# Optimization experiments

Hardware: AMD Instinct MI355X
Metric: run time of the kernel (lower is better)

The kernel has to match this reference:

```python
import jax, jax.numpy as jnp
import numpy as np

NUM_HEADS = 16

def setup_inputs() -> dict:
    key = jax.random.key(0)
    ks = jax.random.split(key, 6)
    b, t, d = 2, 2048, 1024
    s = 0.02
    return {
        "x": jax.random.normal(ks[0], (b, t, d), jnp.float32),
        "Wq": jax.random.normal(ks[1], (d, d), jnp.float32) * s,
        "Wk": jax.random.normal(ks[2], (d, d), jnp.float32) * s,
        "Wv": jax.random.normal(ks[3], (d, d), jnp.float32) * s,
        "Wo": jax.random.normal(ks[4], (d, d), jnp.float32) * s,
        "bo": jnp.zeros((d,), jnp.float32),
    }

def reference(x, Wq, Wk, Wv, Wo, bo):
    b, t, d = x.shape
    h = NUM_HEADS
    hd = d // h  # head_dim = d_out / num_heads
    # torch nn.Linear: y = x @ W.T (qkv_bias=False)
    def split_heads(y):
        return y.reshape(b, t, h, hd).transpose(0, 2, 1, 3)  # [b,h,t,hd]
    q = split_heads(x @ Wq.T)
    k = split_heads(x @ Wk.T)
    v = split_heads(x @ Wv.T)
    scale = 1.0 / jnp.sqrt(jnp.asarray(hd, x.dtype))
    # NOTE: original forward computes but never applies the causal mask or dropout
    scores = jnp.einsum('bhqd,bhkd->bhqk', q, k) * scale
    attn = jax.nn.softmax(scores, axis=-1)
    ctx = jnp.einsum('bhqk,bhkd->bhqd', attn, v)
    ctx = ctx.transpose(0, 2, 1, 3).reshape(b, t, d)
    return ctx @ Wo.T + bo
```

## Files before the change

kernel.cpp:

```cpp
#include <hip/hip_runtime.h>
#include <hip/hip_bf16.h>
#include <math.h>
#include <stdint.h>
#include <string.h>

#define TSEQ 2048
#define DMODEL 1024
#define NH 16
#define HD 64
#define BROWS 4096
#define BH 32

typedef __attribute__((ext_vector_type(8))) short short8;
typedef __attribute__((ext_vector_type(4))) float floatx4;

#define MFMA16 __builtin_amdgcn_mfma_f32_16x16x32_bf16
#define SWZ8(r, q) ((((q) ^ ((r) & 7)) * 8))

#define QSCALE 0.18033688011112042f

__device__ __forceinline__ unsigned short bf16_rne(float f) {
    uint32_t u = __float_as_uint(f);
    u += 0x7FFFu + ((u >> 16) & 1u);
    return (unsigned short)(u >> 16);
}

__device__ __forceinline__ uint32_t pack_bf16x2(float a, float b) {
    __hip_bfloat162 h = __float22bfloat162_rn(float2{a, b});
    uint32_t r;
    memcpy(&r, &h, 4);
    return r;
}

__device__ __forceinline__ void split_bf16(float f, short& hi, short& lo) {
    uint32_t u = __float_as_uint(f);
    hi = (short)(u >> 16);
    float hif = __uint_as_float(u & 0xFFFF0000u);
    lo = (short)bf16_rne(f - hif);
}

__device__ __forceinline__ void async16(const void* g, void* l) {
    __builtin_amdgcn_global_load_lds(
        (__attribute__((address_space(1))) const uint32_t*)g,
        (__attribute__((address_space(3))) uint32_t*)l, 16, 0, 0);
}

struct PackArgs {
    const float4* x;
    ushort4* xb;
    const float4* w[3];
    ushort4* wb[3];
    const float4* wo;
    ushort4* woh;
    ushort4* wol;
};
__global__ __launch_bounds__(256) void pack_all(PackArgs a) {
    const int y = blockIdx.y;
    const int base = blockIdx.x * 256 + threadIdx.x;
    if (y == 0) {
#pragma unroll
        for (int it = 0; it < 4; ++it) {
            int i = base + it * 262144;
            float4 f = a.x[i];
            a.xb[i] = make_ushort4(bf16_rne(f.x), bf16_rne(f.y),
                                   bf16_rne(f.z), bf16_rne(f.w));
        }
    } else if (y <= 3) {
        int w = y - 1;
        float4 f = a.w[w][base];
        a.wb[w][base] = make_ushort4(bf16_rne(f.x), bf16_rne(f.y),
                                     bf16_rne(f.z), bf16_rne(f.w));
    } else {
        float4 f = a.wo[base];
        short h0, l0, h1, l1, h2, l2, h3, l3;
        split_bf16(f.x, h0, l0); split_bf16(f.y, h1, l1);
        split_bf16(f.z, h2, l2); split_bf16(f.w, h3, l3);
        a.woh[base] = make_ushort4(h0, h1, h2, h3);
        a.wol[base] = make_ushort4(l0, l1, l2, l3);
    }
}

#define QSTAGE(DB, K0)                                                          \
    {                                                                           \
        _Pragma("unroll")                                                       \
        for (int j = 0; j < 8; ++j) {                                           \
            int idx = wave * 8 + j;                                             \
            int sub = idx & 15;                                                 \
            const short* s = (idx < 16) ? Asrc : Bsrc;                          \
            short* d = (idx < 16) ? sA[DB] : sB[DB];                            \
            async16(s + (size_t)(sub * 8 + srow) * K + (K0) + soff, d + sub * 512); \
        }                                                                       \
    }

__global__ __launch_bounds__(256) void gemm_qkv(
    const short* __restrict__ Xb,
    const short* __restrict__ Bq, const short* __restrict__ Bk,
    const short* __restrict__ Bv,
    short* __restrict__ Qo, short* __restrict__ Ko, short* __restrict__ Vo) {
    __shared__ short sA[2][128 * 64];
    __shared__ short sB[2][128 * 64];
    const int K = DMODEL;

    const int tid = threadIdx.x;
    const int lane = tid & 63, wave = tid >> 6;
    const int quad = lane >> 4, col = lane & 15;

    const int lin = blockIdx.y * 24 + blockIdx.x;
    const int xcd = lin & 7, j8 = lin >> 3;
    const int bxp = 3 * xcd + (j8 % 3);
    const int byp = j8 / 3;
    const int m0 = byp * 128, n0 = bxp * 128;
    const int which = n0 >> 10;
    const int nn0 = n0 & 1023;
    const int wm = wave >> 1, wn = wave & 1;

    const short* B = (which == 0) ? Bq : (which == 1) ? Bk : Bv;
    const short* Asrc = Xb + (size_t)m0 * K;
    const short* Bsrc = B + (size_t)nn0 * K;

    const int srow = lane >> 3;
    const int soff = (((lane & 7) ^ srow) * 8);

    floatx4 acc[4][4] = {};

    QSTAGE(0, 0);
    for (int t = 0; t < 16; ++t) {
        const int db = t & 1;
        if (t < 15) {
            QSTAGE(db ^ 1, (t + 1) * 64);
            asm volatile("s_waitcnt vmcnt(8)" ::: "memory");
        } else {
            asm volatile("s_waitcnt vmcnt(0)" ::: "memory");
        }
        __builtin_amdgcn_s_barrier();

#pragma unroll
        for (int s2 = 0; s2 < 2; ++s2) {
            short8 a_b[4], b_b[4];
#pragma unroll
            for (int mi = 0; mi < 4; ++mi) {
                int r = wm * 64 + mi * 16 + col;
                a_b[mi] = *(const short8*)&sA[db][r * 64 + SWZ8(r, s2 * 4 + quad)];
            }
#pragma unroll
            for (int ni = 0; ni < 4; ++ni) {
                int r = wn * 64 + ni * 16 + col;
                b_b[ni] = *(const short8*)&sB[db][r * 64 + SWZ8(r, s2 * 4 + quad)];
            }
            __builtin_amdgcn_s_setprio(1);
            if (which == 2) {
#pragma unroll
                for (int mi = 0; mi < 4; ++mi)
#pragma unroll
                    for (int ni = 0; ni < 4; ++ni)
                        acc[mi][ni] = MFMA16(a_b[mi], b_b[ni], acc[mi][ni], 0, 0, 0);
            } else {
#pragma unroll
                for (int mi = 0; mi < 4; ++mi)
#pragma unroll
                    for (int ni = 0; ni < 4; ++ni)
                        acc[mi][ni] = MFMA16(b_b[ni], a_b[mi], acc[mi][ni], 0, 0, 0);
            }
            __builtin_amdgcn_s_setprio(0);
        }
        __builtin_amdgcn_s_barrier();
    }

    const int mb = m0 + wm * 64;
    const int nlb = nn0 + wn * 64;
    if (which == 2) {
#pragma unroll
        for (int ni = 0; ni < 4; ++ni) {
            int n = nlb + ni * 16 + col;
            int h = n >> 6, hd = n & 63;
#pragma unroll
            for (int mi = 0; mi < 4; ++mi) {
                int m4 = mb + mi * 16 + quad * 4;
                int b = m4 >> 11, t0 = m4 & 2047;
                int sw = (t0 & 32) | ((t0 & 12) << 1) | ((t0 & 16) >> 2);
                int tsw = (t0 & ~63) | ((((sw >> 3) ^ (hd & 7)) << 3) | (sw & 7));
                size_t row = ((size_t)(b * NH + h) * HD + hd) * TSEQ;
                *(ushort4*)&Vo[row + tsw] =
                    make_ushort4(bf16_rne(acc[mi][ni][0]), bf16_rne(acc[mi][ni][1]),
                                 bf16_rne(acc[mi][ni][2]), bf16_rne(acc[mi][ni][3]));
            }
        }
    } else {
        short* O = (which == 0) ? Qo : Ko;
        const float sc = (which == 0) ? QSCALE : 1.0f;
#pragma unroll
        for (int mi = 0; mi < 4; ++mi) {
            int m = mb + mi * 16 + col;
            int b = m >> 11, t = m & 2047;
#pragma unroll
            for (int ni = 0; ni < 4; ++ni) {
                int n = nlb + ni * 16 + quad * 4;
                int h = n >> 6, hd = n & 63;
                int hds = (which == 1) ? ((((hd >> 3) ^ (t & 7)) << 3) | (hd & 7)) : hd;
                size_t idx = ((size_t)(b * NH + h) * TSEQ + t) * HD + hds;
                *(ushort4*)&O[idx] =
                    make_ushort4(bf16_rne(acc[mi][ni][0] * sc), bf16_rne(acc[mi][ni][1] * sc),
                                 bf16_rne(acc[mi][ni][2] * sc), bf16_rne(acc[mi][ni][3] * sc));
            }
        }
    }
}

#define QK_U(DB, U, S)                                                          \
    {                                                                           \
        __builtin_amdgcn_s_setprio(1);                                          \
        _Pragma("unroll")                                                       \
        for (int k4 = 0; k4 < 4; ++k4) {                                        \
            short8 kf0 = *(const short8*)(kb0 + (DB) * 8192 + (U) * 4096 + k4 * 1024); \
            short8 kf1 = *(const short8*)(kb1 + (DB) * 8192 + (U) * 4096 + k4 * 1024); \
            S[k4] = MFMA16(kf0, qf[0], S[k4], 0, 0, 0);                         \
            S[k4] = MFMA16(kf1, qf[1], S[k4], 0, 0, 0);                         \
        }                                                                       \
        __builtin_amdgcn_s_setprio(0);                                          \
    }

#define EXPPACK_C(S, C, PFW)                                                    \
    {                                                                           \
        float p0 = __builtin_amdgcn_exp2f(S[2 * (C)][0]);                       \
        float p1 = __builtin_amdgcn_exp2f(S[2 * (C)][1]);                       \
        float p2 = __builtin_amdgcn_exp2f(S[2 * (C)][2]);                       \
        float p3 = __builtin_amdgcn_exp2f(S[2 * (C)][3]);                       \
        float p4 = __builtin_amdgcn_exp2f(S[2 * (C) + 1][0]);                   \
        float p5 = __builtin_amdgcn_exp2f(S[2 * (C) + 1][1]);                   \
        float p6 = __builtin_amdgcn_exp2f(S[2 * (C) + 1][2]);                   \
        float p7 = __builtin_amdgcn_exp2f(S[2 * (C) + 1][3]);                   \
        PFW.w[0] = pack_bf16x2(p0, p1);                                         \
        PFW.w[1] = pack_bf16x2(p2, p3);                                         \
        PFW.w[2] = pack_bf16x2(p4, p5);                                         \
        PFW.w[3] = pack_bf16x2(p6, p7);                                         \
    }

#define PV_C(DB, U, C, PFW)                                                     \
    {                                                                           \
        const short* vbc = (C) ? vb1 : vb0;                                     \
        __builtin_amdgcn_s_setprio(1);                                          \
        lacc = MFMA16(ones.v, PFW.v, lacc, 0, 0, 0);                            \
        _Pragma("unroll")                                                       \
        for (int ni = 0; ni < 4; ++ni) {                                        \
            short8 vf = *(const short8*)(vbc + (DB) * 8192 + (U) * 4096 + ni * 1024); \
            O[ni] = MFMA16(vf, PFW.v, O[ni], 0, 0, 0);                          \
        }                                                                       \
        __builtin_amdgcn_s_setprio(0);                                          \
    }

typedef union { short8 v; uint32_t w[4]; } pfu;

#define ATTN_COMPUTE(DB)                                                        \
    {                                                                           \
        floatx4 sa[4] = {};                                                     \
        QK_U(DB, 0, sa);                                                        \
        pfu pfA0, pfA1;                                                         \
        EXPPACK_C(sa, 0, pfA0);                                                 \
        EXPPACK_C(sa, 1, pfA1);                                                 \
        floatx4 sb[4] = {};                                                     \
        QK_U(DB, 1, sb);                                                        \
              \
        pfu pfB0, pfB1;                                                         \
        PV_C(DB, 0, 0, pfA0);                                                   \
        EXPPACK_C(sb, 0, pfB0);                                                 \
        PV_C(DB, 0, 1, pfA1);                                                   \
        EXPPACK_C(sb, 1, pfB1);                                                 \
        PV_C(DB, 1, 0, pfB0);                                                   \
        PV_C(DB, 1, 1, pfB1);                                                   \
    }

#define ASTAGE(LB)                                                              \
    {                                                                           \
        async16(g0, (LB) + 0 * 512);                                            \
        async16(g1, (LB) + 1 * 512);                                            \
        async16(g2, (LB) + 2 * 512);                                            \
        async16(g3, (LB) + 3 * 512);                                            \
        g0 += ktstep; g1 += ktstep; g2 += ktstep; g3 += ktstep;                 \
    }

__global__ __launch_bounds__(512, 4) void attn_bf16(
    const short* __restrict__ Qb, const short* __restrict__ Kb,
    const short* __restrict__ Vb, short* __restrict__ Cb) {
    __shared__ short sK[2][2][64 * 64];
    __shared__ short sV[2][2][64 * 64];

    const int tid = threadIdx.x;
    const int lane = tid & 63, wave = tid >> 6;
    const int quad = lane >> 4, col = lane & 15;
    const int qt = blockIdx.x, bh = blockIdx.y;
    const size_t bhoff = (size_t)bh * TSEQ * HD;

    const size_t qrow = (size_t)(qt * 128 + wave * 16 + col) * HD;
    short8 qf[2];
#pragma unroll
    for (int c = 0; c < 2; ++c)
        qf[c] = *(const short8*)&Qb[bhoff + qrow + c * 32 + quad * 8];

    const int srow = lane >> 3;
    const int schunk = (lane & 7) * 8;

    const int isV = wave >> 2;
    const int tl = (wave >> 1) & 1;
    const int sb = (wave & 1) * 4;

    const short *g0, *g1, *g2, *g3;
    size_t ktstep;
    if (!isV) {
        g0 = Kb + bhoff + (size_t)(tl * 64 + (sb + 0) * 8 + srow) * HD + schunk;
        g1 = Kb + bhoff + (size_t)(tl * 64 + (sb + 1) * 8 + srow) * HD + schunk;
        g2 = Kb + bhoff + (size_t)(tl * 64 + (sb + 2) * 8 + srow) * HD + schunk;
        g3 = Kb + bhoff + (size_t)(tl * 64 + (sb + 3) * 8 + srow) * HD + schunk;
        ktstep = (size_t)128 * HD;
    } else {
        g0 = Vb + bhoff + (size_t)((sb + 0) * 8 + srow) * TSEQ + tl * 64 + schunk;
        g1 = Vb + bhoff + (size_t)((sb + 1) * 8 + srow) * TSEQ + tl * 64 + schunk;
        g2 = Vb + bhoff + (size_t)((sb + 2) * 8 + srow) * TSEQ + tl * 64 + schunk;
        g3 = Vb + bhoff + (size_t)((sb + 3) * 8 + srow) * TSEQ + tl * 64 + schunk;
        ktstep = 128;
    }
    short* lb0_ = isV ? &sV[0][tl][sb * 512] : &sK[0][tl][sb * 512];
    short* lb1_ = isV ? &sV[1][tl][sb * 512] : &sK[1][tl][sb * 512];

    const int ch0 = ((quad ^ (col & 7)) << 3);
    const int ch1 = (((4 + quad) ^ (col & 7)) << 3);
    const short* kb0 = &sK[0][0][col * 64 + ch0];
    const short* kb1 = &sK[0][0][col * 64 + ch1];
    const short* vb0 = &sV[0][0][col * 64 + ch0];
    const short* vb1 = &sV[0][0][col * 64 + ch1];

    union { short8 v; short s[8]; } ones;
#pragma unroll
    for (int j = 0; j < 8; ++j) ones.s[j] = (short)0x3F80;

    floatx4 lacc = {};
    floatx4 O[4] = {};

    ASTAGE(lb0_);

    for (int kt2 = 0; kt2 < 8; ++kt2) {
        ASTAGE(lb1_);
        asm volatile("s_waitcnt vmcnt(4)" ::: "memory");
        __builtin_amdgcn_s_barrier();
        ATTN_COMPUTE(0);
        __builtin_amdgcn_s_barrier();

        if (kt2 < 7) {
            ASTAGE(lb0_);
            asm volatile("s_waitcnt vmcnt(4)" ::: "memory");
        } else {
            asm volatile("s_waitcnt vmcnt(0)" ::: "memory");
        }
        __builtin_amdgcn_s_barrier();
        ATTN_COMPUTE(1);
        __builtin_amdgcn_s_barrier();
    }

    const float inv = 1.0f / lacc[0];

    const int b = bh >> 4, h = bh & 15;
    const int trow = qt * 128 + wave * 16 + col;
    const size_t obase = (size_t)(b * TSEQ + trow) * DMODEL + h * 64;
#pragma unroll
    for (int ni = 0; ni < 4; ++ni) {
        uint2 pk;
        pk.x = pack_bf16x2(O[ni][0] * inv, O[ni][1] * inv);
        pk.y = pack_bf16x2(O[ni][2] * inv, O[ni][3] * inv);
        *(uint2*)&Cb[obase + ni * 16 + quad * 4] = pk;
    }
}

#define OSTAGE(DB, K0)                                                          \
    {                                                                           \
        _Pragma("unroll")                                                       \
        for (int j = 0; j < 8; ++j) {                                           \
            int idx = wave * 8 + j;                                             \
            int buf = (idx < 16) ? 0 : (idx < 24) ? 1 : 2;                      \
            int sub = (buf == 0) ? idx : (buf == 1) ? idx - 16 : idx - 24;      \
            const short* s = (buf == 0) ? Asrc : (buf == 1) ? Bhsrc : Blsrc;    \
            short* d = (buf == 0) ? sA[DB] : (buf == 1) ? sBh[DB] : sBl[DB];    \
            async16(s + (size_t)(sub * 8 + srow) * K + (K0) + soff, d + sub * 512); \
        }                                                                       \
    }

__global__ __launch_bounds__(256) void gemm_out(
    const short* __restrict__ Ab,
    const short* __restrict__ Bh, const short* __restrict__ Bl,
    const float* __restrict__ bias, float* __restrict__ Of) {
    __shared__ short sA[2][128 * 64];
    __shared__ short sBh[2][64 * 64];
    __shared__ short sBl[2][64 * 64];
    const int K = DMODEL, N = DMODEL;

    const int tid = threadIdx.x;
    const int lane = tid & 63, wave = tid >> 6;
    const int quad = lane >> 4, col = lane & 15;

    const int lin = blockIdx.y * 16 + blockIdx.x;
    const int xcd = lin & 7, j8 = lin >> 3;
    const int bxp = 2 * xcd + (j8 & 1);
    const int byp = j8 >> 1;
    const int m0 = byp * 128, n0 = bxp * 64;
    const int wm = wave >> 1, wn = wave & 1;

    const short* Asrc = Ab + (size_t)m0 * K;
    const short* Bhsrc = Bh + (size_t)n0 * K;
    const short* Blsrc = Bl + (size_t)n0 * K;
    const int srow = lane >> 3;
    const int soff = (((lane & 7) ^ srow) * 8);

    floatx4 acc[4][2] = {};

    OSTAGE(0, 0);
    for (int t = 0; t < 16; ++t) {
        const int db = t & 1;
        if (t < 15) {
            OSTAGE(db ^ 1, (t + 1) * 64);
            asm volatile("s_waitcnt vmcnt(8)" ::: "memory");
        } else {
            asm volatile("s_waitcnt vmcnt(0)" ::: "memory");
        }
        __builtin_amdgcn_s_barrier();

#pragma unroll
        for (int s2 = 0; s2 < 2; ++s2) {
            short8 a_b[4], b_h[2], b_l[2];
#pragma unroll
            for (int mi = 0; mi < 4; ++mi) {
                int r = wm * 64 + mi * 16 + col;
                a_b[mi] = *(const short8*)&sA[db][r * 64 + SWZ8(r, s2 * 4 + quad)];
            }
#pragma unroll
            for (int ni = 0; ni < 2; ++ni) {
                int r = wn * 32 + ni * 16 + col;
                b_h[ni] = *(const short8*)&sBh[db][r * 64 + SWZ8(r, s2 * 4 + quad)];
                b_l[ni] = *(const short8*)&sBl[db][r * 64 + SWZ8(r, s2 * 4 + quad)];
            }
            __builtin_amdgcn_s_setprio(1);
#pragma unroll
            for (int mi = 0; mi < 4; ++mi)
#pragma unroll
                for (int ni = 0; ni < 2; ++ni) {
                    acc[mi][ni] = MFMA16(b_h[ni], a_b[mi], acc[mi][ni], 0, 0, 0);
                    acc[mi][ni] = MFMA16(b_l[ni], a_b[mi], acc[mi][ni], 0, 0, 0);
                }
            __builtin_amdgcn_s_setprio(0);
        }
        __builtin_amdgcn_s_barrier();
    }

    const int mb = m0 + wm * 64, nb = n0 + wn * 32;
#pragma unroll
    for (int mi = 0; mi < 4; ++mi) {
        int m = mb + mi * 16 + col;
#pragma unroll
        for (int ni = 0; ni < 2; ++ni) {
            int n = nb + ni * 16 + quad * 4;
            float4 bv = *(const float4*)&bias[n];
            float4 o = make_float4(acc[mi][ni][0] + bv.x, acc[mi][ni][1] + bv.y,
                                   acc[mi][ni][2] + bv.z, acc[mi][ni][3] + bv.w);
            *(float4*)&Of[(size_t)m * N + n] = o;
        }
    }
}

extern "C" void kernel_launch(void* const* d_in, const int* in_sizes, int n_in,
                              void* d_out, int out_size, void* d_ws, size_t ws_size,
                              hipStream_t stream) {
    const float* x  = (const float*)d_in[0];
    const float* Wq = (const float*)d_in[1];
    const float* Wk = (const float*)d_in[2];
    const float* Wv = (const float*)d_in[3];
    const float* Wo = (const float*)d_in[4];
    const float* bo = (const float*)d_in[5];
    float* out = (float*)d_out;

    const size_t NX = (size_t)BROWS * DMODEL;
    const size_t NW = (size_t)DMODEL * DMODEL;
    short* p = (short*)d_ws;
    short *xb = p;
    short *wqb = xb + NX;
    short *wkb = wqb + NW;
    short *wvb = wkb + NW;
    short *woh = wvb + NW; short *wol = woh + NW;
    short *qb = wol + NW;
    short *kb = qb + NX;
    short *vb = kb + NX;
    short *cb = vb + NX;

    PackArgs pa;
    pa.x = (const float4*)x; pa.xb = (ushort4*)xb;
    pa.w[0] = (const float4*)Wq; pa.wb[0] = (ushort4*)wqb;
    pa.w[1] = (const float4*)Wk; pa.wb[1] = (ushort4*)wkb;
    pa.w[2] = (const float4*)Wv; pa.wb[2] = (ushort4*)wvb;
    pa.wo = (const float4*)Wo; pa.woh = (ushort4*)woh; pa.wol = (ushort4*)wol;
    pack_all<<<dim3(1024, 5), dim3(256), 0, stream>>>(pa);

    gemm_qkv<<<dim3(3 * DMODEL / 128, BROWS / 128), dim3(256), 0, stream>>>(
        xb, wqb, wkb, wvb, qb, kb, vb);

    attn_bf16<<<dim3(TSEQ / 128, BH), dim3(512), 0, stream>>>(qb, kb, vb, cb);

    gemm_out<<<dim3(DMODEL / 64, BROWS / 128), dim3(256), 0, stream>>>(cb, woh, wol, bo, out);
}
```

Before: 186.7 us.

## Load K fragments directly from global memory and stage only V in LDS

The attention kernel stops staging K tiles in shared memory. Each wave now reads its K MFMA fragments straight from global memory into registers, while V keeps its LDS double buffer, now loaded by all eight waves at two chunks each. Block indices are also remapped so that blocks sharing a batch-head land on the same XCD, which should improve L2 reuse of K and V. This cuts LDS traffic and halves LDS use, at the cost of redundant global/L2 K reads across waves, exposed global load latency inside the compute loop, and stricter vmcnt(0) waits that reduce overlap of prefetch with compute.

```diff
diff --git a/kernel.cpp b/kernel.cpp
--- a/kernel.cpp
+++ b/kernel.cpp
@@ -206,18 +206,7 @@
     }
 }
 
-#define QK_U(DB, U, S)                                                          \
-    {                                                                           \
-        __builtin_amdgcn_s_setprio(1);                                          \
-        _Pragma("unroll")                                                       \
-        for (int k4 = 0; k4 < 4; ++k4) {                                        \
-            short8 kf0 = *(const short8*)(kb0 + (DB) * 8192 + (U) * 4096 + k4 * 1024); \
-            short8 kf1 = *(const short8*)(kb1 + (DB) * 8192 + (U) * 4096 + k4 * 1024); \
-            S[k4] = MFMA16(kf0, qf[0], S[k4], 0, 0, 0);                         \
-            S[k4] = MFMA16(kf1, qf[1], S[k4], 0, 0, 0);                         \
-        }                                                                       \
-        __builtin_amdgcn_s_setprio(0);                                          \
-    }
+typedef union { short8 v; uint32_t w[4]; } pfu;
 
 #define EXPPACK_C(S, C, PFW)                                                    \
     {                                                                           \
@@ -248,18 +237,39 @@
         __builtin_amdgcn_s_setprio(0);                                          \
     }
 
-typedef union { short8 v; uint32_t w[4]; } pfu;
-
-#define ATTN_COMPUTE(DB)                                                        \
-    {                                                                           \
+#define KLOAD_U(U, KF)                                                          \
+    {                                                                           \
+        _Pragma("unroll")                                                       \
+        for (int k4 = 0; k4 < 4; ++k4) {                                        \
+            KF[2 * k4]     = *(const short8*)(gk0 + (U) * 4096 + k4 * 1024);    \
+            KF[2 * k4 + 1] = *(const short8*)(gk1 + (U) * 4096 + k4 * 1024);    \
+        }                                                                       \
+    }
+
+#define QK_FROM(KF, S)                                                          \
+    {                                                                           \
+        __builtin_amdgcn_s_setprio(1);                                          \
+        _Pragma("unroll")                                                       \
+        for (int k4 = 0; k4 < 4; ++k4) {                                        \
+            S[k4] = MFMA16(KF[2 * k4], qf[0], S[k4], 0, 0, 0);                  \
+            S[k4] = MFMA16(KF[2 * k4 + 1], qf[1], S[k4], 0, 0, 0);              \
+        }                                                                       \
+        __builtin_amdgcn_s_setprio(0);                                          \
+    }
+
+#define ATTN_COMPUTE_G(DB)                                                      \
+    {                                                                           \
+        short8 ka[8];                                                           \
+        KLOAD_U(0, ka);                                                         \
         floatx4 sa[4] = {};                                                     \
-        QK_U(DB, 0, sa);                                                        \
+        QK_FROM(ka, sa);                                                        \
+        short8 kb_[8];                                                          \
+        KLOAD_U(1, kb_);                 \
         pfu pfA0, pfA1;                                                         \
         EXPPACK_C(sa, 0, pfA0);                                                 \
         EXPPACK_C(sa, 1, pfA1);                                                 \
         floatx4 sb[4] = {};                                                     \
-        QK_U(DB, 1, sb);                                                        \
-              \
+        QK_FROM(kb_, sb);                                                       \
         pfu pfB0, pfB1;                                                         \
         PV_C(DB, 0, 0, pfA0);                                                   \
         EXPPACK_C(sb, 0, pfB0);                                                 \
@@ -269,25 +279,26 @@
         PV_C(DB, 1, 1, pfB1);                                                   \
     }
 
-#define ASTAGE(LB)                                                              \
-    {                                                                           \
-        async16(g0, (LB) + 0 * 512);                                            \
-        async16(g1, (LB) + 1 * 512);                                            \
-        async16(g2, (LB) + 2 * 512);                                            \
-        async16(g3, (LB) + 3 * 512);                                            \
-        g0 += ktstep; g1 += ktstep; g2 += ktstep; g3 += ktstep;                 \
+#define VSTAGE(D0, D1)                                                          \
+    {                                                                           \
+        async16(gv0, D0);                                                       \
+        async16(gv1, D1);                                                       \
+        gv0 += 128; gv1 += 128;                                                 \
     }
 
 __global__ __launch_bounds__(512, 4) void attn_bf16(
     const short* __restrict__ Qb, const short* __restrict__ Kb,
     const short* __restrict__ Vb, short* __restrict__ Cb) {
-    __shared__ short sK[2][2][64 * 64];
-    __shared__ short sV[2][2][64 * 64];
+    __shared__ short sV[2][2][4096];
 
     const int tid = threadIdx.x;
     const int lane = tid & 63, wave = tid >> 6;
     const int quad = lane >> 4, col = lane & 15;
-    const int qt = blockIdx.x, bh = blockIdx.y;
+
+    const int lin = blockIdx.y * 16 + blockIdx.x;
+    const int xcd = lin & 7, j8 = lin >> 3;
+    const int qt = j8 & 15;
+    const int bh = 4 * xcd + (j8 >> 4);
     const size_t bhoff = (size_t)bh * TSEQ * HD;
 
     const size_t qrow = (size_t)(qt * 128 + wave * 16 + col) * HD;
@@ -299,32 +310,21 @@
     const int srow = lane >> 3;
     const int schunk = (lane & 7) * 8;
 
-    const int isV = wave >> 2;
-    const int tl = (wave >> 1) & 1;
-    const int sb = (wave & 1) * 4;
-
-    const short *g0, *g1, *g2, *g3;
-    size_t ktstep;
-    if (!isV) {
-        g0 = Kb + bhoff + (size_t)(tl * 64 + (sb + 0) * 8 + srow) * HD + schunk;
-        g1 = Kb + bhoff + (size_t)(tl * 64 + (sb + 1) * 8 + srow) * HD + schunk;
-        g2 = Kb + bhoff + (size_t)(tl * 64 + (sb + 2) * 8 + srow) * HD + schunk;
-        g3 = Kb + bhoff + (size_t)(tl * 64 + (sb + 3) * 8 + srow) * HD + schunk;
-        ktstep = (size_t)128 * HD;
-    } else {
-        g0 = Vb + bhoff + (size_t)((sb + 0) * 8 + srow) * TSEQ + tl * 64 + schunk;
-        g1 = Vb + bhoff + (size_t)((sb + 1) * 8 + srow) * TSEQ + tl * 64 + schunk;
-        g2 = Vb + bhoff + (size_t)((sb + 2) * 8 + srow) * TSEQ + tl * 64 + schunk;
-        g3 = Vb + bhoff + (size_t)((sb + 3) * 8 + srow) * TSEQ + tl * 64 + schunk;
-        ktstep = 128;
-    }
-    short* lb0_ = isV ? &sV[0][tl][sb * 512] : &sK[0][tl][sb * 512];
-    short* lb1_ = isV ? &sV[1][tl][sb * 512] : &sK[1][tl][sb * 512];
+    const int n0_ = wave * 2, n1_ = n0_ + 1;
+    const int tl0 = n0_ >> 3, sb0 = n0_ & 7;
+    const int tl1 = n1_ >> 3, sb1 = n1_ & 7;
+    const short* gv0 = Vb + bhoff + (size_t)(sb0 * 8 + srow) * TSEQ + tl0 * 64 + schunk;
+    const short* gv1 = Vb + bhoff + (size_t)(sb1 * 8 + srow) * TSEQ + tl1 * 64 + schunk;
+    short* vd0_0 = &sV[0][tl0][sb0 * 512];
+    short* vd0_1 = &sV[0][tl1][sb1 * 512];
+    short* vd1_0 = &sV[1][tl0][sb0 * 512];
+    short* vd1_1 = &sV[1][tl1][sb1 * 512];
 
     const int ch0 = ((quad ^ (col & 7)) << 3);
     const int ch1 = (((4 + quad) ^ (col & 7)) << 3);
-    const short* kb0 = &sK[0][0][col * 64 + ch0];
-    const short* kb1 = &sK[0][0][col * 64 + ch1];
+    const short* gk0 = Kb + bhoff + col * HD + ch0;
+    const short* gk1 = Kb + bhoff + col * HD + ch1;
+
     const short* vb0 = &sV[0][0][col * 64 + ch0];
     const short* vb1 = &sV[0][0][col * 64 + ch1];
 
@@ -335,23 +335,23 @@
     floatx4 lacc = {};
     floatx4 O[4] = {};
 
-    ASTAGE(lb0_);
+    VSTAGE(vd0_0, vd0_1);
+    asm volatile("s_waitcnt vmcnt(0)" ::: "memory");
+    __builtin_amdgcn_s_barrier();
 
     for (int kt2 = 0; kt2 < 8; ++kt2) {
-        ASTAGE(lb1_);
-        asm volatile("s_waitcnt vmcnt(4)" ::: "memory");
+        VSTAGE(vd1_0, vd1_1);
+        ATTN_COMPUTE_G(0);
+        gk0 += 8192; gk1 += 8192;
+        asm volatile("s_waitcnt vmcnt(0)" ::: "memory");
         __builtin_amdgcn_s_barrier();
-        ATTN_COMPUTE(0);
-        __builtin_amdgcn_s_barrier();
 
         if (kt2 < 7) {
-            ASTAGE(lb0_);
-            asm volatile("s_waitcnt vmcnt(4)" ::: "memory");
-        } else {
-            asm volatile("s_waitcnt vmcnt(0)" ::: "memory");
-        }
-        __builtin_amdgcn_s_barrier();
-        ATTN_COMPUTE(1);
+            VSTAGE(vd0_0, vd0_1);
+        }
+        ATTN_COMPUTE_G(1);
+        gk0 += 8192; gk1 += 8192;
+        asm volatile("s_waitcnt vmcnt(0)" ::: "memory");
         __builtin_amdgcn_s_barrier();
     }
 
```

Result: slower. 201.3 us (+7.8%).
